# Kernel tuning notes

Measured on AMD Instinct MI355X. Metric: run time of the kernel, lower is better.

## Reference

```python
import jax, jax.numpy as jnp
import numpy as np

B, N, C = 8192, 4, 1024
H = 16
D = C // H              # head_dim = 64
P = 4                   # proj_dim (Linformer reduced length)
IDX_I, IDX_J = 1, 2     # Return_attn_way(use_cls=True, attn_selet_way=0)
SCALE = D ** -0.5


def setup_inputs() -> dict:
    key = jax.random.key(0)
    ks = jax.random.split(key, 6)
    std = 0.02
    x = jax.random.normal(ks[0], (B, N, C), dtype=jnp.float32)
    W_qkv = jax.random.normal(ks[1], (C, 3 * C), dtype=jnp.float32) * std   # qkv_bias=False
    W_proj = jax.random.normal(ks[2], (C, C), dtype=jnp.float32) * std
    b_proj = jnp.zeros((C,), dtype=jnp.float32)
    W_E = jax.random.normal(ks[3], (P, N), dtype=jnp.float32) * std         # torch Linear weight [out,in]
    W_F = jax.random.normal(ks[4], (P, N), dtype=jnp.float32) * std
    return {"x": x, "W_qkv": W_qkv, "W_proj": W_proj, "b_proj": b_proj,
            "W_E": W_E, "W_F": W_F}


def reference(x, W_qkv, W_proj, b_proj, W_E, W_F):
    b, n, c = x.shape
    # qkv projection -> [B,N,3,H,D] -> q,k,v each [B,H,N,D]
    qkv = (x @ W_qkv).reshape(b, n, 3, H, D)
    qkv = jnp.transpose(qkv, (2, 0, 3, 1, 4))
    q, k, v = qkv[0], qkv[1], qkv[2]
    q = q * SCALE  # q_norm/k_norm are Identity (qk_norm=False)

    # gathered single-token score: q[:,:,IDX_I,:] @ k[:,:,IDX_J,:].T -> [B,H,H]
    # (torch transpose(-2,-1) on the [B,H,D] slice swaps H and D)
    attn_sel = jnp.einsum('bhd,bgd->bhg', q[:, :, IDX_I, :], k[:, :, IDX_J, :])
    attn_sel_sig = jax.nn.sigmoid(attn_sel)

    # Linformer E/F projection along the sequence axis: [B,H,N,D] -> [B,H,P,D]
    k_low = jnp.einsum('bhnd,pn->bhpd', k, W_E)
    v_low = jnp.einsum('bhnd,pn->bhpd', v, W_F)

    # reduced softmax attention: [B,H,N,P]
    attn = jnp.einsum('bhnd,bhpd->bhnp', q, k_low)
    attn = jax.nn.softmax(attn, axis=-1)  # attn_drop is identity (p=0, eval)
    out = jnp.einsum('bhnp,bhpd->bhnd', attn, v_low)

    # merge heads and output projection
    out = jnp.transpose(out, (0, 2, 1, 3)).reshape(b, n, c)
    out = out @ W_proj.T + b_proj  # proj_drop identity
    return (out, attn_sel_sig)
```

## Files before the change

### kernel.cpp

```cpp
#include <hip/hip_runtime.h>
#include <hip/hip_bf16.h>

#define B_   8192
#define SEQ_ 4
#define C_   1024
#define H_   16
#define D_   64
#define P_   4
#define M_   (B_ * SEQ_)
#define K_   1024
#define N1_  3072

typedef __attribute__((ext_vector_type(8))) short short8;
typedef __attribute__((ext_vector_type(4))) float f32x4;

__device__ __forceinline__ unsigned short f2bf(float f) {
  union { float f; unsigned u; } v; v.f = f;
  unsigned r = v.u + 0x7fffu + ((v.u >> 16) & 1u);
  return (unsigned short)(r >> 16);
}
__device__ __forceinline__ float bf2f(unsigned short u) {
  union { unsigned u; float f; } v; v.u = ((unsigned)u) << 16;
  return v.f;
}

__global__ __launch_bounds__(256) void cast_bf16_k(const float* __restrict__ in,
                                                   unsigned short* __restrict__ out) {
  int i = blockIdx.x * 256 + threadIdx.x;
  float4 v = ((const float4*)in)[i];
  ushort4 o;
  o.x = f2bf(v.x); o.y = f2bf(v.y); o.z = f2bf(v.z); o.w = f2bf(v.w);
  ((ushort4*)out)[i] = o;
}

__global__ __launch_bounds__(256) void transpose_wqkv_k(const float* __restrict__ in,
                                                        unsigned short* __restrict__ out) {
  __shared__ float t[32][33];
  int tx = threadIdx.x, ty = threadIdx.y;
  int j0 = blockIdx.x * 32, c0 = blockIdx.y * 32;
#pragma unroll
  for (int i = 0; i < 4; ++i)
    t[ty + i * 8][tx] = in[(size_t)(c0 + ty + i * 8) * N1_ + j0 + tx];
  __syncthreads();
#pragma unroll
  for (int i = 0; i < 4; ++i) {
    int j = j0 + ty + i * 8;
    float v = t[tx][ty + i * 8];
    if (j < 1024) v *= 0.125f;
    out[(size_t)j * K_ + c0 + tx] = f2bf(v);
  }
}

template <int OUTMODE>
__global__ __launch_bounds__(256) void gemm_nt(const unsigned short* __restrict__ A,
                                               const unsigned short* __restrict__ Bm,
                                               unsigned short* __restrict__ Cbf,
                                               float* __restrict__ Cf,
                                               const float* __restrict__ bias,
                                               int K, int Ncols) {
  __shared__ unsigned short lsA[128 * 32];
  __shared__ unsigned short lsB[128 * 32];
  const int tid = threadIdx.x;
  const int wave = tid >> 6, lane = tid & 63;
  const int wm = (wave >> 1) * 64, wn = (wave & 1) * 64;
  const long tile_m = (long)blockIdx.y * 128, tile_n = (long)blockIdx.x * 128;

  f32x4 acc[4][4] = {};

  const int ci0 = (wave * 2 + 0) * 64 + lane;
  const int ci1 = (wave * 2 + 1) * 64 + lane;
  const int r0 = ci0 >> 2, kc0 = (ci0 & 3) * 8;
  const int r1 = ci1 >> 2, kc1 = (ci1 & 3) * 8;
  const unsigned short* gA0 = A + (tile_m + r0) * K + kc0;
  const unsigned short* gA1 = A + (tile_m + r1) * K + kc1;
  const unsigned short* gB0 = Bm + (tile_n + r0) * K + kc0;
  const unsigned short* gB1 = Bm + (tile_n + r1) * K + kc1;
  unsigned short* dA0 = lsA + (wave * 2 + 0) * 512;
  unsigned short* dA1 = lsA + (wave * 2 + 1) * 512;
  unsigned short* dB0 = lsB + (wave * 2 + 0) * 512;
  unsigned short* dB1 = lsB + (wave * 2 + 1) * 512;

  const int r16 = lane & 15, q8 = (lane >> 4) * 8;

  for (int kt = 0; kt < K; kt += 32) {
    __builtin_amdgcn_global_load_lds((const __attribute__((address_space(1))) void*)(gA0 + kt),
                                     (__attribute__((address_space(3))) void*)dA0, 16, 0, 0);
    __builtin_amdgcn_global_load_lds((const __attribute__((address_space(1))) void*)(gA1 + kt),
                                     (__attribute__((address_space(3))) void*)dA1, 16, 0, 0);
    __builtin_amdgcn_global_load_lds((const __attribute__((address_space(1))) void*)(gB0 + kt),
                                     (__attribute__((address_space(3))) void*)dB0, 16, 0, 0);
    __builtin_amdgcn_global_load_lds((const __attribute__((address_space(1))) void*)(gB1 + kt),
                                     (__attribute__((address_space(3))) void*)dB1, 16, 0, 0);
    __syncthreads();

    short8 afr[4], bfr[4];
#pragma unroll
    for (int mi = 0; mi < 4; ++mi)
      afr[mi] = *(const short8*)&lsA[(wm + mi * 16 + r16) * 32 + q8];
#pragma unroll
    for (int ni = 0; ni < 4; ++ni)
      bfr[ni] = *(const short8*)&lsB[(wn + ni * 16 + r16) * 32 + q8];
#pragma unroll
    for (int mi = 0; mi < 4; ++mi)
#pragma unroll
      for (int ni = 0; ni < 4; ++ni)
        acc[mi][ni] = __builtin_amdgcn_mfma_f32_16x16x32_bf16(afr[mi], bfr[ni], acc[mi][ni], 0, 0, 0);
    __syncthreads();
  }

  const int cl = lane & 15, rq = (lane >> 4) * 4;
#pragma unroll
  for (int mi = 0; mi < 4; ++mi)
#pragma unroll
    for (int ni = 0; ni < 4; ++ni) {
      long col = tile_n + wn + ni * 16 + cl;
      float bv = (OUTMODE == 1) ? bias[col] : 0.f;
#pragma unroll
      for (int r = 0; r < 4; ++r) {
        long row = tile_m + wm + mi * 16 + rq + r;
        if (OUTMODE == 0)
          Cbf[(size_t)row * Ncols + col] = f2bf(acc[mi][ni][r]);
        else
          Cf[(size_t)row * Ncols + col] = acc[mi][ni][r] + bv;
      }
    }
}

__global__ __launch_bounds__(256) void attn_mfma_k(const unsigned short* __restrict__ qkv,
                                                   const float* __restrict__ WE,
                                                   const float* __restrict__ WF,
                                                   unsigned short* __restrict__ hmid,
                                                   float* __restrict__ attn_sel) {
  __shared__ float As[4][16 * 17 + 2];
  const int tid = threadIdx.x;
  const int wave = tid >> 6, lane = tid & 63;
  const int b = blockIdx.x * 4 + wave;
  const size_t qb = (size_t)b * 4 * N1_;

  const int hl = lane & 15;
  const int qg = lane >> 4;

  f32x4 accS[4][4] = {};
#pragma unroll
  for (int ch = 0; ch < 2; ++ch) {
    const int off = ch * 32 + qg * 8;
    short8 qf[4], kf[4];
#pragma unroll
    for (int n = 0; n < 4; ++n)
      qf[n] = *(const short8*)(qkv + qb + (size_t)n * N1_ + 0 + hl * 64 + off);
#pragma unroll
    for (int m = 0; m < 4; ++m)
      kf[m] = *(const short8*)(qkv + qb + (size_t)m * N1_ + 1024 + hl * 64 + off);
#pragma unroll
    for (int n = 0; n < 4; ++n)
#pragma unroll
      for (int m = 0; m < 4; ++m)
        accS[n][m] = __builtin_amdgcn_mfma_f32_16x16x32_bf16(qf[n], kf[m], accS[n][m], 0, 0, 0);
  }

#pragma unroll
  for (int r = 0; r < 4; ++r) {
    float t = accS[1][2][r];
    attn_sel[(size_t)b * 256 + (qg * 4 + r) * 16 + hl] = 1.f / (1.f + __expf(-t));
  }

  if ((hl >> 2) == qg) {
    const int h = hl, rr = h & 3;
    float Sm[4][4];
#pragma unroll
    for (int n = 0; n < 4; ++n)
#pragma unroll
      for (int m = 0; m < 4; ++m) Sm[n][m] = accS[n][m][rr];
#pragma unroll
    for (int n = 0; n < 4; ++n) {
      float lg[4];
#pragma unroll
      for (int p = 0; p < 4; ++p)
        lg[p] = Sm[n][0] * WE[p * 4] + Sm[n][1] * WE[p * 4 + 1] +
                Sm[n][2] * WE[p * 4 + 2] + Sm[n][3] * WE[p * 4 + 3];
      float mx = fmaxf(fmaxf(lg[0], lg[1]), fmaxf(lg[2], lg[3]));
      float e0 = __expf(lg[0] - mx), e1 = __expf(lg[1] - mx);
      float e2 = __expf(lg[2] - mx), e3 = __expf(lg[3] - mx);
      float inv = 1.f / (e0 + e1 + e2 + e3);
      e0 *= inv; e1 *= inv; e2 *= inv; e3 *= inv;
#pragma unroll
      for (int m = 0; m < 4; ++m)
        As[wave][h * 17 + n * 4 + m] =
            e0 * WF[0 * 4 + m] + e1 * WF[1 * 4 + m] + e2 * WF[2 * 4 + m] + e3 * WF[3 * 4 + m];
    }
  }
  __syncthreads();

  {
    const int h = lane & 15, dg = lane >> 4;
    float Ap[4][4];
#pragma unroll
    for (int n = 0; n < 4; ++n)
#pragma unroll
      for (int m = 0; m < 4; ++m) Ap[n][m] = As[wave][h * 17 + n * 4 + m];

    float outv[4][16] = {};
#pragma unroll
    for (int m = 0; m < 4; ++m) {
      const unsigned short* vp = qkv + qb + (size_t)m * N1_ + 2048 + h * 64 + dg * 16;
      short8 v0 = *(const short8*)(vp);
      short8 v1 = *(const short8*)(vp + 8);
      float vf[16];
#pragma unroll
      for (int j = 0; j < 8; ++j) {
        vf[j] = bf2f((unsigned short)v0[j]);
        vf[8 + j] = bf2f((unsigned short)v1[j]);
      }
#pragma unroll
      for (int n = 0; n < 4; ++n)
#pragma unroll
        for (int d = 0; d < 16; ++d) outv[n][d] += Ap[n][m] * vf[d];
    }
#pragma unroll
    for (int n = 0; n < 4; ++n) {
      short8 o0, o1;
#pragma unroll
      for (int j = 0; j < 8; ++j) {
        o0[j] = (short)f2bf(outv[n][j]);
        o1[j] = (short)f2bf(outv[n][8 + j]);
      }
      unsigned short* op = hmid + ((size_t)b * 4 + n) * C_ + h * 64 + dg * 16;
      *(short8*)(op) = o0;
      *(short8*)(op + 8) = o1;
    }
  }
}

extern "C" void kernel_launch(void* const* d_in, const int* in_sizes, int n_in,
                              void* d_out, int out_size, void* d_ws, size_t ws_size,
                              hipStream_t stream) {
  (void)in_sizes; (void)n_in; (void)out_size; (void)ws_size;
  const float* x      = (const float*)d_in[0];
  const float* W_qkv  = (const float*)d_in[1];
  const float* W_proj = (const float*)d_in[2];
  const float* b_proj = (const float*)d_in[3];
  const float* W_E    = (const float*)d_in[4];
  const float* W_F    = (const float*)d_in[5];

  float* out0 = (float*)d_out;
  float* out1 = out0 + (size_t)M_ * C_;

  char* ws = (char*)d_ws;
  unsigned short* x_bf   = (unsigned short*)(ws);
  unsigned short* wqkvT  = (unsigned short*)(ws + 67108864);
  unsigned short* wproj  = (unsigned short*)(ws + 73400320);
  unsigned short* qkv_bf = (unsigned short*)(ws + 75497472);
  unsigned short* hmid   = x_bf;

  cast_bf16_k<<<(M_ * C_) / 1024, 256, 0, stream>>>(x, x_bf);
  transpose_wqkv_k<<<dim3(N1_ / 32, C_ / 32), dim3(32, 8), 0, stream>>>(W_qkv, wqkvT);
  cast_bf16_k<<<(C_ * C_) / 1024, 256, 0, stream>>>(W_proj, wproj);

  gemm_nt<0><<<dim3(N1_ / 128, M_ / 128), 256, 0, stream>>>(x_bf, wqkvT, qkv_bf, nullptr,
                                                            nullptr, K_, N1_);
  attn_mfma_k<<<B_ / 4, 256, 0, stream>>>(qkv_bf, W_E, W_F, hmid, out1);

  gemm_nt<1><<<dim3(C_ / 128, M_ / 128), 256, 0, stream>>>(hmid, wproj, nullptr, out0,
                                                           b_proj, K_, C_);
}
```

Baseline: 662.9 us.

## Switch main GEMMs to FP8 scaled MFMA with bf16 fixup for selected tokens

Both large GEMMs (the QKV projection and the output projection) now take FP8 operands and use the scaled 16x16x128 f8f6f4 MFMA with fixed power-of-two scales, which halves operand bytes and raises matrix throughput. A separate bf16 GEMM recomputes q at token 1 and k at token 2, so the attn_sel output keeps higher precision. The attention kernel now writes FP8 activations for the output projection. In exchange there are extra conversion kernels and a fixup GEMM, and FP8 quantization error with fixed scales may hurt accuracy of the main output.

```diff
diff --git a/kernel.cpp b/kernel.cpp
--- a/kernel.cpp
+++ b/kernel.cpp
@@ -2,17 +2,15 @@
 #include <hip/hip_bf16.h>
 
 #define B_   8192
-#define SEQ_ 4
 #define C_   1024
 #define H_   16
-#define D_   64
-#define P_   4
-#define M_   (B_ * SEQ_)
+#define M_   (B_ * 4)
 #define K_   1024
 #define N1_  3072
 
 typedef __attribute__((ext_vector_type(8))) short short8;
 typedef __attribute__((ext_vector_type(4))) float f32x4;
+typedef __attribute__((ext_vector_type(8))) int   int8v;
 
 __device__ __forceinline__ unsigned short f2bf(float f) {
   union { float f; unsigned u; } v; v.f = f;
@@ -23,18 +21,30 @@
   union { unsigned u; float f; } v; v.u = ((unsigned)u) << 16;
   return v.f;
 }
-
-__global__ __launch_bounds__(256) void cast_bf16_k(const float* __restrict__ in,
-                                                   unsigned short* __restrict__ out) {
-  int i = blockIdx.x * 256 + threadIdx.x;
-  float4 v = ((const float4*)in)[i];
-  ushort4 o;
-  o.x = f2bf(v.x); o.y = f2bf(v.y); o.z = f2bf(v.z); o.w = f2bf(v.w);
-  ((ushort4*)out)[i] = o;
+__device__ __forceinline__ int pk_fp8(float a, float b, float c, float d) {
+  int r = __builtin_amdgcn_cvt_pk_fp8_f32(a, b, 0, false);
+  r = __builtin_amdgcn_cvt_pk_fp8_f32(c, d, r, true);
+  return r;
+}
+
+__global__ __launch_bounds__(256) void cast_x_k(const float* __restrict__ x,
+                                                unsigned char* __restrict__ x8,
+                                                unsigned short* __restrict__ xsel) {
+  const int row = blockIdx.x;
+  const int tid = threadIdx.x;
+  float4 v = ((const float4*)(x + (size_t)row * 1024))[tid];
+  ((int*)(x8 + (size_t)row * 1024))[tid] = pk_fp8(v.x, v.y, v.z, v.w);
+  const int n = row & 3;
+  if (n == 1 || n == 2) {
+    ushort4 o;
+    o.x = f2bf(v.x); o.y = f2bf(v.y); o.z = f2bf(v.z); o.w = f2bf(v.w);
+    ((ushort4*)(xsel + ((size_t)(n - 1) * 8192 + (row >> 2)) * 1024))[tid] = o;
+  }
 }
 
 __global__ __launch_bounds__(256) void transpose_wqkv_k(const float* __restrict__ in,
-                                                        unsigned short* __restrict__ out) {
+                                                        unsigned short* __restrict__ outb,
+                                                        unsigned char* __restrict__ out8) {
   __shared__ float t[32][33];
   int tx = threadIdx.x, ty = threadIdx.y;
   int j0 = blockIdx.x * 32, c0 = blockIdx.y * 32;
@@ -47,26 +57,32 @@
     int j = j0 + ty + i * 8;
     float v = t[tx][ty + i * 8];
     if (j < 1024) v *= 0.125f;
-    out[(size_t)j * K_ + c0 + tx] = f2bf(v);
-  }
-}
-
-template <int OUTMODE>
-__global__ __launch_bounds__(256) void gemm_nt(const unsigned short* __restrict__ A,
-                                               const unsigned short* __restrict__ Bm,
-                                               unsigned short* __restrict__ Cbf,
-                                               float* __restrict__ Cf,
-                                               const float* __restrict__ bias,
-                                               int K, int Ncols) {
+    outb[(size_t)j * K_ + c0 + tx] = f2bf(v);
+    out8[(size_t)j * K_ + c0 + tx] =
+        (unsigned char)(__builtin_amdgcn_cvt_pk_fp8_f32(v * 32.f, v * 32.f, 0, false) & 0xff);
+  }
+}
+
+__global__ __launch_bounds__(256) void cast_wproj_k(const float* __restrict__ in,
+                                                    unsigned char* __restrict__ out) {
+  int i = blockIdx.x * 256 + threadIdx.x;
+  float4 v = ((const float4*)in)[i];
+  ((int*)out)[i] = pk_fp8(v.x * 32.f, v.y * 32.f, v.z * 32.f, v.w * 32.f);
+}
+
+__global__ __launch_bounds__(256) void gemm_fixup(const unsigned short* __restrict__ A,
+                                                  const unsigned short* __restrict__ B0,
+                                                  unsigned short* __restrict__ Cbf) {
   __shared__ unsigned short lsA[128 * 32];
   __shared__ unsigned short lsB[128 * 32];
+  const int K = 1024, Ncols = 1024;
   const int tid = threadIdx.x;
   const int wave = tid >> 6, lane = tid & 63;
   const int wm = (wave >> 1) * 64, wn = (wave & 1) * 64;
   const long tile_m = (long)blockIdx.y * 128, tile_n = (long)blockIdx.x * 128;
+  const unsigned short* Bm = B0 + (tile_m >= 8192 ? (size_t)1024 * 1024 : 0);
 
   f32x4 acc[4][4] = {};
-
   const int ci0 = (wave * 2 + 0) * 64 + lane;
   const int ci1 = (wave * 2 + 1) * 64 + lane;
   const int r0 = ci0 >> 2, kc0 = (ci0 & 3) * 8;
@@ -79,7 +95,6 @@
   unsigned short* dA1 = lsA + (wave * 2 + 1) * 512;
   unsigned short* dB0 = lsB + (wave * 2 + 0) * 512;
   unsigned short* dB1 = lsB + (wave * 2 + 1) * 512;
-
   const int r16 = lane & 15, q8 = (lane >> 4) * 8;
 
   for (int kt = 0; kt < K; kt += 32) {
@@ -92,7 +107,6 @@
     __builtin_amdgcn_global_load_lds((const __attribute__((address_space(1))) void*)(gB1 + kt),
                                      (__attribute__((address_space(3))) void*)dB1, 16, 0, 0);
     __syncthreads();
-
     short8 afr[4], bfr[4];
 #pragma unroll
     for (int mi = 0; mi < 4; ++mi)
@@ -105,6 +119,88 @@
 #pragma unroll
       for (int ni = 0; ni < 4; ++ni)
         acc[mi][ni] = __builtin_amdgcn_mfma_f32_16x16x32_bf16(afr[mi], bfr[ni], acc[mi][ni], 0, 0, 0);
+    __syncthreads();
+  }
+  const int cl = lane & 15, rq = (lane >> 4) * 4;
+#pragma unroll
+  for (int mi = 0; mi < 4; ++mi)
+#pragma unroll
+    for (int ni = 0; ni < 4; ++ni) {
+      long col = tile_n + wn + ni * 16 + cl;
+#pragma unroll
+      for (int r = 0; r < 4; ++r) {
+        long row = tile_m + wm + mi * 16 + rq + r;
+        Cbf[(size_t)row * Ncols + col] = f2bf(acc[mi][ni][r]);
+      }
+    }
+}
+
+template <int OUTMODE>
+__global__ __launch_bounds__(256) void gemm_mx(const unsigned char* __restrict__ A,
+                                               const unsigned char* __restrict__ Bm,
+                                               unsigned short* __restrict__ Cbf,
+                                               float* __restrict__ Cf,
+                                               const float* __restrict__ bias,
+                                               int K, int Ncols, int sA, int sB) {
+  __shared__ unsigned char lsA[16384];
+  __shared__ unsigned char lsB[16384];
+  const int tid = threadIdx.x;
+  const int wave = tid >> 6, lane = tid & 63;
+  const int wm = (wave >> 1) * 64, wn = (wave & 1) * 64;
+  const long tile_m = (long)blockIdx.y * 128, tile_n = (long)blockIdx.x * 128;
+
+  f32x4 acc[4][4] = {};
+
+  size_t offA[4], offB[4];
+#pragma unroll
+  for (int j = 0; j < 4; ++j) {
+    int ci = j * 256 + tid;
+    int qg = ci >> 8, id = ci & 255;
+    int r2 = (id >> 3) & 1, r3 = (id >> 4) & 1;
+    int rr0 = ((id >> 1) & 1) ^ r2, rr1 = ((id >> 2) & 1) ^ r3;
+    int row = rr0 | (rr1 << 1) | (r2 << 2) | (r3 << 3) | ((id >> 5) << 4);
+    int half = (id & 1) ^ rr0;
+    offA[j] = (size_t)(tile_m + row) * K + qg * 32 + half * 16;
+    offB[j] = (size_t)(tile_n + row) * K + qg * 32 + half * 16;
+  }
+
+  const int hl = lane & 15, qg = lane >> 4;
+  const int swz = (hl & 12) << 3;
+  const int laneFragBase = qg * 4096 + ((hl * 32) ^ swz) + ((hl & 1) << 4);
+
+  for (int kt = 0; kt < K; kt += 128) {
+#pragma unroll
+    for (int j = 0; j < 4; ++j) {
+      __builtin_amdgcn_global_load_lds(
+          (const __attribute__((address_space(1))) void*)(A + offA[j] + kt),
+          (__attribute__((address_space(3))) void*)(lsA + (j * 256 + wave * 64) * 16), 16, 0, 0);
+      __builtin_amdgcn_global_load_lds(
+          (const __attribute__((address_space(1))) void*)(Bm + offB[j] + kt),
+          (__attribute__((address_space(3))) void*)(lsB + (j * 256 + wave * 64) * 16), 16, 0, 0);
+    }
+    __syncthreads();
+
+    int8v af[4], bfr[4];
+#pragma unroll
+    for (int mi = 0; mi < 4; ++mi) {
+      int ad = (wm + mi * 16) * 32 + laneFragBase;
+      int4 h0 = *(const int4*)(lsA + ad);
+      int4 h1 = *(const int4*)(lsA + (ad ^ 16));
+      af[mi] = int8v{h0.x, h0.y, h0.z, h0.w, h1.x, h1.y, h1.z, h1.w};
+    }
+#pragma unroll
+    for (int ni = 0; ni < 4; ++ni) {
+      int ad = (wn + ni * 16) * 32 + laneFragBase;
+      int4 h0 = *(const int4*)(lsB + ad);
+      int4 h1 = *(const int4*)(lsB + (ad ^ 16));
+      bfr[ni] = int8v{h0.x, h0.y, h0.z, h0.w, h1.x, h1.y, h1.z, h1.w};
+    }
+#pragma unroll
+    for (int mi = 0; mi < 4; ++mi)
+#pragma unroll
+      for (int ni = 0; ni < 4; ++ni)
+        acc[mi][ni] = __builtin_amdgcn_mfma_scale_f32_16x16x128_f8f6f4(
+            af[mi], bfr[ni], acc[mi][ni], 0, 0, 0, sA, 0, sB);
     __syncthreads();
   }
 
@@ -127,20 +223,21 @@
 }
 
 __global__ __launch_bounds__(256) void attn_mfma_k(const unsigned short* __restrict__ qkv,
+                                                   const unsigned short* __restrict__ q1,
+                                                   const unsigned short* __restrict__ k2,
                                                    const float* __restrict__ WE,
                                                    const float* __restrict__ WF,
-                                                   unsigned short* __restrict__ hmid,
+                                                   unsigned char* __restrict__ hmid8,
                                                    float* __restrict__ attn_sel) {
   __shared__ float As[4][16 * 17 + 2];
   const int tid = threadIdx.x;
   const int wave = tid >> 6, lane = tid & 63;
   const int b = blockIdx.x * 4 + wave;
   const size_t qb = (size_t)b * 4 * N1_;
-
-  const int hl = lane & 15;
-  const int qg = lane >> 4;
+  const int hl = lane & 15, qg = lane >> 4;
 
   f32x4 accS[4][4] = {};
+  f32x4 accSel = {};
 #pragma unroll
   for (int ch = 0; ch < 2; ++ch) {
     const int off = ch * 32 + qg * 8;
@@ -156,13 +253,14 @@
 #pragma unroll
       for (int m = 0; m < 4; ++m)
         accS[n][m] = __builtin_amdgcn_mfma_f32_16x16x32_bf16(qf[n], kf[m], accS[n][m], 0, 0, 0);
-  }
-
-#pragma unroll
-  for (int r = 0; r < 4; ++r) {
-    float t = accS[1][2][r];
-    attn_sel[(size_t)b * 256 + (qg * 4 + r) * 16 + hl] = 1.f / (1.f + __expf(-t));
-  }
+    short8 qs = *(const short8*)(q1 + (size_t)b * 1024 + hl * 64 + off);
+    short8 ks = *(const short8*)(k2 + (size_t)b * 1024 + hl * 64 + off);
+    accSel = __builtin_amdgcn_mfma_f32_16x16x32_bf16(qs, ks, accSel, 0, 0, 0);
+  }
+
+#pragma unroll
+  for (int r = 0; r < 4; ++r)
+    attn_sel[(size_t)b * 256 + (qg * 4 + r) * 16 + hl] = 1.f / (1.f + __expf(-accSel[r]));
 
   if ((hl >> 2) == qg) {
     const int h = hl, rr = h & 3;
@@ -218,15 +316,11 @@
     }
 #pragma unroll
     for (int n = 0; n < 4; ++n) {
-      short8 o0, o1;
-#pragma unroll
-      for (int j = 0; j < 8; ++j) {
-        o0[j] = (short)f2bf(outv[n][j]);
-        o1[j] = (short)f2bf(outv[n][8 + j]);
-      }
-      unsigned short* op = hmid + ((size_t)b * 4 + n) * C_ + h * 64 + dg * 16;
-      *(short8*)(op) = o0;
-      *(short8*)(op + 8) = o1;
+      int w0 = pk_fp8(outv[n][0] * 32.f, outv[n][1] * 32.f, outv[n][2] * 32.f, outv[n][3] * 32.f);
+      int w1 = pk_fp8(outv[n][4] * 32.f, outv[n][5] * 32.f, outv[n][6] * 32.f, outv[n][7] * 32.f);
+      int w2 = pk_fp8(outv[n][8] * 32.f, outv[n][9] * 32.f, outv[n][10] * 32.f, outv[n][11] * 32.f);
+      int w3 = pk_fp8(outv[n][12] * 32.f, outv[n][13] * 32.f, outv[n][14] * 32.f, outv[n][15] * 32.f);
+      *(int4*)(hmid8 + ((size_t)b * 4 + n) * 1024 + h * 64 + dg * 16) = make_int4(w0, w1, w2, w3);
     }
   }
 }
@@ -246,20 +340,27 @@
   float* out1 = out0 + (size_t)M_ * C_;
 
   char* ws = (char*)d_ws;
-  unsigned short* x_bf   = (unsigned short*)(ws);
-  unsigned short* wqkvT  = (unsigned short*)(ws + 67108864);
-  unsigned short* wproj  = (unsigned short*)(ws + 73400320);
-  unsigned short* qkv_bf = (unsigned short*)(ws + 75497472);
-  unsigned short* hmid   = x_bf;
-
-  cast_bf16_k<<<(M_ * C_) / 1024, 256, 0, stream>>>(x, x_bf);
-  transpose_wqkv_k<<<dim3(N1_ / 32, C_ / 32), dim3(32, 8), 0, stream>>>(W_qkv, wqkvT);
-  cast_bf16_k<<<(C_ * C_) / 1024, 256, 0, stream>>>(W_proj, wproj);
-
-  gemm_nt<0><<<dim3(N1_ / 128, M_ / 128), 256, 0, stream>>>(x_bf, wqkvT, qkv_bf, nullptr,
-                                                            nullptr, K_, N1_);
-  attn_mfma_k<<<B_ / 4, 256, 0, stream>>>(qkv_bf, W_E, W_F, hmid, out1);
-
-  gemm_nt<1><<<dim3(C_ / 128, M_ / 128), 256, 0, stream>>>(hmid, wproj, nullptr, out0,
-                                                           b_proj, K_, C_);
-}
+  unsigned short* xsel   = (unsigned short*)(ws);
+  unsigned short* wqkvTb = (unsigned short*)(ws + 33554432);
+  unsigned short* qkv_bf = (unsigned short*)(ws);
+  unsigned char*  x8     = (unsigned char*)(ws + 201326592);
+  unsigned char*  hmid8  = x8;
+  unsigned char*  wqkvT8 = (unsigned char*)(ws + 234881024);
+  unsigned char*  wproj8 = (unsigned char*)(ws + 238026752);
+  unsigned short* q1k2   = (unsigned short*)(ws + 239075328);
+
+  cast_x_k<<<32768, 256, 0, stream>>>(x, x8, xsel);
+  transpose_wqkv_k<<<dim3(96, 32), dim3(32, 8), 0, stream>>>(W_qkv, wqkvTb, wqkvT8);
+  cast_wproj_k<<<1024, 256, 0, stream>>>(W_proj, wproj8);
+
+  gemm_fixup<<<dim3(8, 128), 256, 0, stream>>>(xsel, wqkvTb, q1k2);
+
+  gemm_mx<0><<<dim3(24, 256), 256, 0, stream>>>(x8, wqkvT8, qkv_bf, nullptr, nullptr,
+                                                1024, 3072, 127, 122);
+
+  attn_mfma_k<<<B_ / 4, 256, 0, stream>>>(qkv_bf, q1k2, q1k2 + (size_t)8192 * 1024,
+                                          W_E, W_F, hmid8, out1);
+
+  gemm_mx<1><<<dim3(8, 256), 256, 0, stream>>>(hmid8, wproj8, nullptr, out0, b_proj,
+                                               1024, 1024, 122, 122);
+}
```

Result: faster. 577.4 us (-12.9%).
